# Kernel optimization log

Measured on AMD Instinct MI355X. Metric: run time of the kernel, lower is better.

## Reference

```python
import jax, jax.numpy as jnp
import numpy as np
import math
from jax.scipy.special import gammaln

B, H, W = 32, 960, 960
BLOCK = 96  # official NIQE/NRQM block size

# AGGD shape-parameter lookup table (same grid as torch impl: 0.2..10 step 0.001)
_GAM_NP = np.arange(0.2, 10.0 + 1e-6, 0.001, dtype=np.float64)
_RG_NP = np.array([math.exp(2.0 * math.lgamma(2.0 / g) - math.lgamma(1.0 / g) - math.lgamma(3.0 / g)) for g in _GAM_NP], dtype=np.float32)
GAM = jnp.asarray(_GAM_NP.astype(np.float32))
RGAM = jnp.asarray(_RG_NP)

def _gauss_kernel(size, sigma):
    ax = np.arange(size, dtype=np.float64) - (size - 1) / 2.0
    xx, yy = np.meshgrid(ax, ax)
    k = np.exp(-(xx ** 2 + yy ** 2) / (2.0 * sigma ** 2))
    return (k / k.sum()).astype(np.float32)

K7 = jnp.asarray(_gauss_kernel(7, 7.0 / 6.0))[None, None]  # MSCN window
K3 = jnp.asarray(_gauss_kernel(3, 0.5))[None, None]        # pyramid / downsample kernel

def _conv_same(x, k, edge_pad):
    ph = k.shape[-1] // 2
    mode = 'edge' if edge_pad else 'constant'
    x = jnp.pad(x, ((0, 0), (0, 0), (ph, ph), (ph, ph)), mode=mode)
    return jax.lax.conv_general_dilated(x, k, (1, 1), 'VALID', dimension_numbers=('NCHW', 'OIHW', 'NCHW'))

def _normalize(img):
    # MSCN: (img - mu) / (sigma + 1), replicate padding
    mu = _conv_same(img, K7, True)
    sigma = jnp.sqrt(jnp.abs(_conv_same(img * img, K7, True) - mu * mu))
    return (img - mu) / (sigma + 1.0)

def _downsample(img):
    # gaussian blur (3x3, sigma 0.5, zero same-pad) + stride-2 decimation
    return _conv_same(img, K3, False)[:, :, ::2, ::2]

def _aggd(x):
    # x: [b, nb, h, w]; vectorized AGGD parameter estimation over all blocks
    hw = (-2, -1)
    x2 = x * x
    ml = (x < 0).astype(x.dtype)
    mr = (x > 0).astype(x.dtype)
    cl = jnp.maximum(ml.sum(hw), 1.0)
    cr = jnp.maximum(mr.sum(hw), 1.0)
    lstd = jnp.sqrt((x2 * ml).sum(hw) / cl)
    rstd = jnp.sqrt((x2 * mr).sum(hw) / cr)
    gh = lstd / jnp.maximum(rstd, 1e-12)
    rhat = jnp.mean(jnp.abs(x), hw) ** 2 / jnp.maximum(jnp.mean(x2, hw), 1e-12)
    rhn = rhat * (gh ** 3 + 1.0) * (gh + 1.0) / ((gh * gh + 1.0) ** 2)
    idx = jnp.argmin(jnp.abs(RGAM - rhn[..., None]), axis=-1)  # table lookup
    alpha = GAM[idx]
    conv = jnp.exp(0.5 * (gammaln(1.0 / alpha) - gammaln(3.0 / alpha)))
    return alpha, lstd * conv, rstd * conv

def _features(blocks):
    # 18 features per block: AGGD of block + AGGD of 4 shifted products
    alpha, bl, br = _aggd(blocks)
    feats = [alpha, (bl + br) / 2.0]
    for shift in ((0, 1), (1, 0), (1, 1), (1, -1)):
        sb = jnp.roll(blocks, shift, axis=(2, 3))
        a, l, r = _aggd(blocks * sb)
        mean = (r - l) * jnp.exp(gammaln(2.0 / a) - gammaln(1.0 / a))
        feats += [a, mean, l, r]
    return jnp.stack(feats, axis=-1)  # [b, nb, 18]

def _blocks(x, bs):
    b, _, h, w = x.shape
    nh, nw = h // bs, w // bs
    x = x[:, 0].reshape(b, nh, bs, nw, bs).transpose(0, 1, 3, 2, 4)
    return x.reshape(b, nh * nw, bs, bs)

def setup_inputs() -> dict:
    key = jax.random.key(0)
    k1, k2, k3 = jax.random.split(key, 3)
    X = jax.random.uniform(k1, (B, 1, H, W), jnp.float32) * 255.0
    mu_pris = jax.random.normal(k2, (36,), jnp.float32)
    A = jax.random.normal(k3, (36, 36), jnp.float32)
    cov_pris = A @ A.T / 36.0 + jnp.eye(36, dtype=jnp.float32)  # SPD pristine covariance
    return {"X": X, "mu_pris": mu_pris, "cov_pris": cov_pris}

def reference(X, mu_pris, cov_pris):
    feats = []
    img = X
    for scale in (1, 2):
        xn = _normalize(img)
        feats.append(_features(_blocks(xn, BLOCK // scale)))  # [b, 100, 18]
        if scale == 1:
            img = _downsample(img)
    d = jnp.concatenate(feats, axis=-1)  # [b, nb, 36]
    mu_dist = d.mean(axis=1)  # [b, 36]
    c = d - mu_dist[:, None, :]
    cov_dist = jnp.einsum('bnf,bng->bfg', c, c) / (d.shape[1] - 1)
    invcov = jnp.linalg.pinv((cov_pris[None] + cov_dist) / 2.0)
    diff = mu_pris[None] - mu_dist
    q = jnp.einsum('bf,bfg,bg->b', diff, invcov, diff)
    return jnp.sqrt(jnp.maximum(q, 0.0))
```

## Files before the change

### kernel.cpp

```cpp
#include <hip/hip_runtime.h>
#include <hip/hip_fp16.h>
#include <math.h>

#define NTAB 9801
typedef unsigned int uint;

struct WParams { float w1[7]; float wd[3]; };

__device__ inline __half2 u2h2(uint u) { return __builtin_bit_cast(__half2, u); }
__device__ inline uint h22u(__half2 h) { return __builtin_bit_cast(uint, h); }
__device__ inline float flo(uint u) { return __low2float(u2h2(u)); }
__device__ inline float fhi(uint u) { return __high2float(u2h2(u)); }
__device__ inline uint pkmul(uint a, uint b) { return h22u(__hmul2(u2h2(a), u2h2(b))); }
__device__ inline uint pack2(float a, float b) {
    return h22u(__halves2half2(__float2half(a), __float2half(b)));
}
__device__ inline uint algn16(uint hi, uint lo) {
    return (uint)((((unsigned long long)hi << 32) | lo) >> 16);
}
typedef _Float16 h2v __attribute__((ext_vector_type(2)));
__device__ inline float fdot2f(uint a, uint b, float c) {
#if defined(__has_builtin) && __has_builtin(__builtin_amdgcn_fdot2)
    return __builtin_amdgcn_fdot2(__builtin_bit_cast(h2v, a), __builtin_bit_cast(h2v, b), c, false);
#else
    return c + flo(a) * flo(b) + fhi(a) * fhi(b);
#endif
}

template <int S, bool FUSE_DOWN, bool TABLES, typename TIN>
__global__ __launch_bounds__(256) void mscn_col_k(const TIN* __restrict__ src,
                                                  uint* __restrict__ xn_out,
                                                  __half* __restrict__ down_out,
                                                  WParams wp,
                                                  float* __restrict__ rgam,
                                                  float* __restrict__ gam) {
    constexpr int ROW_W = 132, H_IN = 34, H_OUT = 28;
    constexpr int NTX = (S + 255) / 256, NTY = (S + H_OUT - 1) / H_OUT;
    constexpr int NBLK = 32 * NTX * NTY;

    if constexpr (TABLES) {
        if (blockIdx.x >= (unsigned)NBLK) {
            int i = (blockIdx.x - NBLK) * 256 + threadIdx.x;
            if (i < NTAB) {
                double g = 0.2 + (double)i * 0.001;
                double v = exp(2.0 * lgamma(2.0 / g) - lgamma(1.0 / g) - lgamma(3.0 / g));
                rgam[i] = (float)v;
                gam[i]  = (float)g;
            }
            return;
        }
    }

    __shared__ uint tin[ROW_W * H_IN];

    const int tid = threadIdx.x;
    const int bid = blockIdx.x;
    const int b  = bid / (NTX * NTY);
    const int t2 = bid % (NTX * NTY);
    const int x0 = min((t2 / NTY) * 256, S - 256);
    const int y0 = min((t2 % NTY) * H_OUT, S - H_OUT);

    const float* w1 = wp.w1;
    uint wA[4], wB[4];
    wA[0] = pack2(w1[0], w1[1]); wA[1] = pack2(w1[2], w1[3]);
    wA[2] = pack2(w1[4], w1[5]); wA[3] = pack2(w1[6], 0.f);
    wB[0] = pack2(0.f, w1[0]);   wB[1] = pack2(w1[1], w1[2]);
    wB[2] = pack2(w1[3], w1[4]); wB[3] = pack2(w1[5], w1[6]);

    const TIN* img = src + (size_t)b * S * S;
    for (int i = tid; i < ROW_W * H_IN; i += 256) {
        int r = i / ROW_W, w = i - r * ROW_W;
        int gy = y0 + r - 3; gy = gy < 0 ? 0 : (gy >= S ? S - 1 : gy);
        int c0 = x0 + 2 * w - 3; c0 = c0 < 0 ? 0 : (c0 >= S ? S - 1 : c0);
        int c1 = (x0 + 2 * w - 2) < 0 ? 0 : ((x0 + 2 * w - 2) >= S ? S - 1 : x0 + 2 * w - 2);
        const TIN* rp = img + (size_t)gy * S;
        tin[i] = pack2((float)rp[c0], (float)rp[c1]);
    }
    __syncthreads();

    const int g = tid >> 7, c = tid & 127;
    const int R0 = g * 14;

    auto horiz = [&](int row, float& s1A, float& s2A, float& s1B, float& s2B) {
        const uint* pw = &tin[row * ROW_W + c];
        uint q0 = pw[0], q1 = pw[1], q2 = pw[2], q3 = pw[3];
        uint p0 = pkmul(q0, q0), p1 = pkmul(q1, q1), p2 = pkmul(q2, q2), p3 = pkmul(q3, q3);
        s1A = fdot2f(q3, wA[3], fdot2f(q2, wA[2], fdot2f(q1, wA[1], fdot2f(q0, wA[0], 0.f))));
        s2A = fdot2f(p3, wA[3], fdot2f(p2, wA[2], fdot2f(p1, wA[1], fdot2f(p0, wA[0], 0.f))));
        s1B = fdot2f(q3, wB[3], fdot2f(q2, wB[2], fdot2f(q1, wB[1], fdot2f(q0, wB[0], 0.f))));
        s2B = fdot2f(p3, wB[3], fdot2f(p2, wB[2], fdot2f(p1, wB[1], fdot2f(p0, wB[0], 0.f))));
    };

    float r1A[7], r2A[7], r1B[7], r2B[7];
#pragma unroll
    for (int ir = 0; ir < 6; ir++) horiz(R0 + ir, r1A[ir], r2A[ir], r1B[ir], r2B[ir]);

    uint* xnp = xn_out + ((((size_t)b * S + y0 + R0) * S + x0) >> 1) + c;
#pragma unroll
    for (int u = 0; u < 14; u++) {
        horiz(R0 + u + 6, r1A[(u + 6) % 7], r2A[(u + 6) % 7], r1B[(u + 6) % 7], r2B[(u + 6) % 7]);
        float s1a = 0.f, s2a = 0.f, s1b = 0.f, s2b = 0.f;
#pragma unroll
        for (int dy = 0; dy < 7; dy++) {
            s1a += w1[dy] * r1A[(u + dy) % 7];  s2a += w1[dy] * r2A[(u + dy) % 7];
            s1b += w1[dy] * r1B[(u + dy) % 7];  s2b += w1[dy] * r2B[(u + dy) % 7];
        }
        int row = R0 + u + 3;
        uint cw1 = tin[row * ROW_W + c + 1], cw2 = tin[row * ROW_W + c + 2];
        float v0a = fhi(cw1), v0b = flo(cw2);
        float xa = (v0a - s1a) / (sqrtf(fabsf(s2a - s1a * s1a)) + 1.f);
        float xb = (v0b - s1b) / (sqrtf(fabsf(s2b - s1b * s1b)) + 1.f);
        xnp[(size_t)u * (S / 2)] = pack2(xa, xb);
    }

    if constexpr (FUSE_DOWN) {
        const float* wd = wp.wd;
        const int d = tid & 127, hf = tid >> 7;
        const int Xd = x0 / 2 + d;
        const float mL = (x0 + 2 * d - 1 >= 0) ? 1.f : 0.f;
#pragma unroll
        for (int jj = 0; jj < 7; jj++) {
            int j = hf * 7 + jj;
            int Yd = y0 / 2 + j;
            float acc = 0.f;
#pragma unroll
            for (int a = 0; a < 3; a++) {
                int gy = 2 * Yd - 1 + a;
                if (gy < 0) continue;
                int tr = gy - y0 + 3;
                uint u1 = tin[tr * ROW_W + d + 1];
                uint u2 = tin[tr * ROW_W + d + 2];
                float rs = wd[0] * flo(u1) * mL + wd[1] * fhi(u1) + wd[2] * flo(u2);
                acc += wd[a] * rs;
            }
            down_out[((size_t)b * (S / 2) + Yd) * (S / 2) + Xd] = __float2half(acc);
        }
    }
}

template <int BS>
__global__ __launch_bounds__(256) void feat2_k(const __half* __restrict__ xnimg, int S,
                                               const float* __restrict__ rgam,
                                               const float* __restrict__ gam,
                                               float* __restrict__ dfeat, int foff) {
    constexpr int WROW = BS / 2;
    constexpr int NWORD = BS * BS / 2;
    constexpr int NITER = (NWORD + 255) / 256;
    __shared__ uint xs[NWORD];
    __shared__ float red[4 * 20];
    __shared__ float tot[20];

    const int tid = threadIdx.x;
    const int b   = blockIdx.x / 100;
    const int blk = blockIdx.x % 100;
    const int by  = (blk / 10) * BS;
    const int bx  = (blk % 10) * BS;

    const uint* gw = (const uint*)xnimg;
    for (int i = tid; i < NWORD; i += 256) {
        int y = i / WROW, w = i - y * WROW;
        xs[i] = gw[((((size_t)b * S + by + y) * S + bx) >> 1) + w];
    }
    __syncthreads();

    float ssq[5], sab[5], ssg[5];
    uint  cnt[5];
#pragma unroll
    for (int v = 0; v < 5; v++) { ssq[v] = sab[v] = ssg[v] = 0.f; cnt[v] = 0u; }

    const uint ONE2 = 0x3C003C00u;

    for (int k = 0; k < NITER; k++) {
        int idx = tid + k * 256;
        if (idx * 2 < BS * BS) {
            int p0 = idx * 2;
            int y = p0 / BS;
            int x = p0 - y * BS;
            int w0i = x >> 1;
            int wm = w0i ? w0i - 1 : WROW - 1;
            int wp = (w0i + 1 == WROW) ? 0 : w0i + 1;
            int ym1 = y ? y - 1 : BS - 1;
            int rb = y * WROW, rbm = ym1 * WROW;
            uint V0 = xs[rb + w0i];
            uint WL = xs[rb + wm];
            uint AL = xs[rbm + wm];
            uint AC = xs[rbm + w0i];
            uint AR = xs[rbm + wp];
            uint vv[5];
            vv[0] = V0;
            vv[1] = pkmul(V0, algn16(V0, WL));
            vv[2] = pkmul(V0, AC);
            vv[3] = pkmul(V0, algn16(AC, AL));
            vv[4] = pkmul(V0, algn16(AR, AC));
#pragma unroll
            for (int v = 0; v < 5; v++) {
                uint av = vv[v] & 0x7FFF7FFFu;
                ssq[v] = fdot2f(vv[v], vv[v], ssq[v]);
                sab[v] = fdot2f(av, ONE2, sab[v]);
                ssg[v] = fdot2f(vv[v], av, ssg[v]);
                cnt[v] += (vv[v] >> 15) & 0x00010001u;
            }
        }
    }

    const int wid = tid >> 6, lane = tid & 63;
#pragma unroll
    for (int v = 0; v < 5; v++) {
        float a = ssq[v], bb = sab[v], cc = ssg[v];
        float dd = (float)((cnt[v] & 0xFFFFu) + (cnt[v] >> 16));
        for (int off = 32; off >= 1; off >>= 1) {
            a += __shfl_down(a, off); bb += __shfl_down(bb, off);
            cc += __shfl_down(cc, off); dd += __shfl_down(dd, off);
        }
        if (lane == 0) {
            red[wid * 20 + v]      = a;
            red[wid * 20 + 5 + v]  = bb;
            red[wid * 20 + 10 + v] = cc;
            red[wid * 20 + 15 + v] = dd;
        }
    }
    __syncthreads();
    if (tid < 20) tot[tid] = red[tid] + red[20 + tid] + red[40 + tid] + red[60 + tid];
    __syncthreads();

    if (tid < 5) {
        const int v = tid;
        const float N = (float)(BS * BS);
        float ssqv = tot[v], sabv = tot[5 + v], ssgv = tot[10 + v], clv = tot[15 + v];
        float sql = fmaxf(0.5f * (ssqv - ssgv), 0.f);
        float sqr = fmaxf(0.5f * (ssqv + ssgv), 0.f);
        float cl = fmaxf(clv, 1.f), cr = fmaxf(N - clv, 1.f);
        float lstd = sqrtf(sql / cl), rstd = sqrtf(sqr / cr);
        float gh = lstd / fmaxf(rstd, 1e-12f);
        float mabs = sabv / N, msq = ssqv / N;
        float rhat = (mabs * mabs) / fmaxf(msq, 1e-12f);
        float gh2 = gh * gh;
        float target = rhat * (gh * gh2 + 1.f) * (gh + 1.f) / ((gh2 + 1.f) * (gh2 + 1.f));

        int lo = 0, hi = NTAB - 1, j = NTAB;
        while (lo <= hi) {
            int mid = (lo + hi) >> 1;
            if (rgam[mid] >= target) { j = mid; hi = mid - 1; } else lo = mid + 1;
        }
        int i0 = j > 0 ? j - 1 : 0;
        int i1 = j < NTAB ? j : NTAB - 1;
        float d0 = fabsf(rgam[i0] - target);
        float d1 = fabsf(rgam[i1] - target);
        int bi = (d1 < d0) ? i1 : i0;

        float alpha = gam[bi];
        float conv  = expf(0.5f * (lgammaf(1.f / alpha) - lgammaf(3.f / alpha)));
        float bl = lstd * conv, br = rstd * conv;
        float* outp = dfeat + ((size_t)b * 100 + blk) * 36 + foff;
        if (v == 0) {
            outp[0] = alpha;
            outp[1] = 0.5f * (bl + br);
        } else {
            float mean = (br - bl) * expf(lgammaf(2.f / alpha) - lgammaf(1.f / alpha));
            int base = 2 + (v - 1) * 4;
            outp[base + 0] = alpha; outp[base + 1] = mean;
            outp[base + 2] = bl;    outp[base + 3] = br;
        }
    }
}

__global__ __launch_bounds__(256) void final_k(const float* __restrict__ dfeat,
                                               const float* __restrict__ mu_pris,
                                               const float* __restrict__ cov_pris,
                                               float* __restrict__ out) {
    __shared__ float  ds[3600];
    __shared__ float  mu[36];
    __shared__ double M[36][37];
    __shared__ double rhs[36];
    __shared__ double qacc;
    const int b = blockIdx.x, tid = threadIdx.x;
    const float* src = dfeat + (size_t)b * 3600;
    for (int i = tid; i < 3600; i += 256) ds[i] = src[i];
    __syncthreads();
    if (tid < 36) {
        float s = 0.f;
        for (int n = 0; n < 100; n++) s += ds[n * 36 + tid];
        mu[tid] = s / 100.f;
    }
    __syncthreads();
    for (int i = tid; i < 3600; i += 256) ds[i] -= mu[i % 36];
    if (tid < 36) rhs[tid] = (double)mu_pris[tid] - (double)mu[tid];
    if (tid == 0) qacc = 0.0;
    __syncthreads();
    for (int e = tid; e < 1296; e += 256) {
        int f = e / 36, g = e % 36;
        float s = 0.f;
        for (int n = 0; n < 100; n++) s += ds[n * 36 + f] * ds[n * 36 + g];
        M[f][g] = 0.5 * ((double)cov_pris[e] + (double)(s / 99.f));
    }
    __syncthreads();
    for (int j = 0; j < 36; j++) {
        if (tid == 0) qacc += rhs[j] * rhs[j] / M[j][j];
        int i = j + 1 + tid;
        if (i < 36) {
            double L = M[i][j] / M[j][j];
            for (int k = j; k < 36; k++) M[i][k] -= L * M[j][k];
            rhs[i] -= L * rhs[j];
        }
        __syncthreads();
    }
    if (tid == 0) out[b] = sqrtf((float)(qacc > 0.0 ? qacc : 0.0));
}

static WParams make_weights() {
    WParams p;
    double wt[7], s = 0.0; const double sg = 7.0 / 6.0;
    for (int i = 0; i < 7; i++) { double d = i - 3; wt[i] = exp(-d * d / (2.0 * sg * sg)); s += wt[i]; }
    for (int i = 0; i < 7; i++) p.w1[i] = (float)(wt[i] / s);
    double e1 = exp(-2.0), sd = 1.0 + 2.0 * e1;
    p.wd[0] = p.wd[2] = (float)(e1 / sd);
    p.wd[1] = (float)(1.0 / sd);
    return p;
}

extern "C" void kernel_launch(void* const* d_in, const int* in_sizes, int n_in,
                              void* d_out, int out_size, void* d_ws, size_t ws_size,
                              hipStream_t stream) {
    const float* X        = (const float*)d_in[0];
    const float* mu_pris  = (const float*)d_in[1];
    const float* cov_pris = (const float*)d_in[2];
    float* out = (float*)d_out;

    char* ws = (char*)d_ws;
    float*  rgam   = (float*)(ws);
    float*  gam    = (float*)(ws + 39424);
    float*  dfeat  = (float*)(ws + 78848);
    __half* xn960  = (__half*)(ws + 539648);
    __half* img480 = (__half*)(ws + 59522048);
    __half* xn480  = (__half*)(ws + 74267648);

    WParams wp = make_weights();

    constexpr int NB960 = 32 * 4 * 35;
    constexpr int TBLB  = (NTAB + 255) / 256;
    mscn_col_k<960, true,  true,  float ><<<NB960 + TBLB, 256, 0, stream>>>(
        X, (uint*)xn960, img480, wp, rgam, gam);
    mscn_col_k<480, false, false, __half><<<32 * 36, 256, 0, stream>>>(
        img480, (uint*)xn480, nullptr, wp, rgam, gam);
    feat2_k<96><<<3200, 256, 0, stream>>>(xn960, 960, rgam, gam, dfeat, 0);
    feat2_k<48><<<3200, 256, 0, stream>>>(xn480, 480, rgam, gam, dfeat, 18);
    final_k<<<32, 256, 0, stream>>>(dfeat, mu_pris, cov_pris, out);
}
```

Before: 236.7 us.

## Enlarge MSCN row tiles, vectorize interior loads, use packed float2 and rcp

After: 223.2 us. -5.7%, faster.

```diff
diff --git a/kernel.cpp b/kernel.cpp
--- a/kernel.cpp
+++ b/kernel.cpp
@@ -4,37 +4,34 @@
 
 #define NTAB 9801
 typedef unsigned int uint;
+typedef float f2v __attribute__((ext_vector_type(2)));
+typedef _Float16 h2v __attribute__((ext_vector_type(2)));
 
 struct WParams { float w1[7]; float wd[3]; };
 
 __device__ inline __half2 u2h2(uint u) { return __builtin_bit_cast(__half2, u); }
-__device__ inline uint h22u(__half2 h) { return __builtin_bit_cast(uint, h); }
 __device__ inline float flo(uint u) { return __low2float(u2h2(u)); }
 __device__ inline float fhi(uint u) { return __high2float(u2h2(u)); }
-__device__ inline uint pkmul(uint a, uint b) { return h22u(__hmul2(u2h2(a), u2h2(b))); }
+__device__ inline uint pkmul(uint a, uint b) { return __builtin_bit_cast(uint, __hmul2(u2h2(a), u2h2(b))); }
 __device__ inline uint pack2(float a, float b) {
-    return h22u(__halves2half2(__float2half(a), __float2half(b)));
+    return __builtin_bit_cast(uint, __builtin_amdgcn_cvt_pkrtz(a, b));
 }
 __device__ inline uint algn16(uint hi, uint lo) {
     return (uint)((((unsigned long long)hi << 32) | lo) >> 16);
 }
-typedef _Float16 h2v __attribute__((ext_vector_type(2)));
 __device__ inline float fdot2f(uint a, uint b, float c) {
-#if defined(__has_builtin) && __has_builtin(__builtin_amdgcn_fdot2)
     return __builtin_amdgcn_fdot2(__builtin_bit_cast(h2v, a), __builtin_bit_cast(h2v, b), c, false);
-#else
-    return c + flo(a) * flo(b) + fhi(a) * fhi(b);
-#endif
-}
+}
+__device__ inline float rcpf(float x) { return __builtin_amdgcn_rcpf(x); }
 
 template <int S, bool FUSE_DOWN, bool TABLES, typename TIN>
-__global__ __launch_bounds__(256) void mscn_col_k(const TIN* __restrict__ src,
-                                                  uint* __restrict__ xn_out,
-                                                  __half* __restrict__ down_out,
-                                                  WParams wp,
-                                                  float* __restrict__ rgam,
-                                                  float* __restrict__ gam) {
-    constexpr int ROW_W = 132, H_IN = 34, H_OUT = 28;
+__global__ __launch_bounds__(256, 6) void mscn_col_k(const TIN* __restrict__ src,
+                                                     uint* __restrict__ xn_out,
+                                                     __half* __restrict__ down_out,
+                                                     WParams wp,
+                                                     float* __restrict__ rgam,
+                                                     float* __restrict__ gam) {
+    constexpr int ROW_W = 132, H_OUT = 42, H_IN = H_OUT + 6, RPT = H_OUT / 2;
     constexpr int NTX = (S + 255) / 256, NTY = (S + H_OUT - 1) / H_OUT;
     constexpr int NBLK = 32 * NTX * NTY;
 
@@ -62,54 +59,69 @@
 
     const float* w1 = wp.w1;
     uint wA[4], wB[4];
-    wA[0] = pack2(w1[0], w1[1]); wA[1] = pack2(w1[2], w1[3]);
-    wA[2] = pack2(w1[4], w1[5]); wA[3] = pack2(w1[6], 0.f);
-    wB[0] = pack2(0.f, w1[0]);   wB[1] = pack2(w1[1], w1[2]);
-    wB[2] = pack2(w1[3], w1[4]); wB[3] = pack2(w1[5], w1[6]);
+    wA[0] = pack2(0.f, w1[0]);   wA[1] = pack2(w1[1], w1[2]);
+    wA[2] = pack2(w1[3], w1[4]); wA[3] = pack2(w1[5], w1[6]);
+    wB[0] = pack2(w1[0], w1[1]); wB[1] = pack2(w1[2], w1[3]);
+    wB[2] = pack2(w1[4], w1[5]); wB[3] = pack2(w1[6], 0.f);
 
     const TIN* img = src + (size_t)b * S * S;
-    for (int i = tid; i < ROW_W * H_IN; i += 256) {
-        int r = i / ROW_W, w = i - r * ROW_W;
-        int gy = y0 + r - 3; gy = gy < 0 ? 0 : (gy >= S ? S - 1 : gy);
-        int c0 = x0 + 2 * w - 3; c0 = c0 < 0 ? 0 : (c0 >= S ? S - 1 : c0);
-        int c1 = (x0 + 2 * w - 2) < 0 ? 0 : ((x0 + 2 * w - 2) >= S ? S - 1 : x0 + 2 * w - 2);
-        const TIN* rp = img + (size_t)gy * S;
-        tin[i] = pack2((float)rp[c0], (float)rp[c1]);
+    const bool interior = (x0 >= 4) && (x0 <= S - 260) && (y0 >= 3) && (y0 <= S - H_IN + 3);
+
+    if (interior && sizeof(TIN) == 4) {
+        const float4* base = reinterpret_cast<const float4*>((const float*)img + (size_t)(y0 - 3) * S + (x0 - 4));
+        const int f4row = S / 4;
+        for (int i = tid; i < 66 * H_IN; i += 256) {
+            int r = i / 66, k = i - r * 66;
+            float4 v = base[(size_t)r * f4row + k];
+            tin[r * ROW_W + 2 * k]     = pack2(v.x, v.y);
+            tin[r * ROW_W + 2 * k + 1] = pack2(v.z, v.w);
+        }
+    } else {
+        for (int i = tid; i < ROW_W * H_IN; i += 256) {
+            int r = i / ROW_W, w = i - r * ROW_W;
+            int gy = y0 + r - 3; gy = gy < 0 ? 0 : (gy >= S ? S - 1 : gy);
+            int c0 = x0 - 4 + 2 * w; c0 = c0 < 0 ? 0 : (c0 >= S ? S - 1 : c0);
+            int c1 = x0 - 3 + 2 * w; c1 = c1 < 0 ? 0 : (c1 >= S ? S - 1 : c1);
+            const TIN* rp = img + (size_t)gy * S;
+            tin[i] = pack2((float)rp[c0], (float)rp[c1]);
+        }
     }
     __syncthreads();
 
     const int g = tid >> 7, c = tid & 127;
-    const int R0 = g * 14;
-
-    auto horiz = [&](int row, float& s1A, float& s2A, float& s1B, float& s2B) {
+    const int R0 = g * RPT;
+
+    auto horiz = [&](int row, f2v& o1, f2v& o2) {
         const uint* pw = &tin[row * ROW_W + c];
-        uint q0 = pw[0], q1 = pw[1], q2 = pw[2], q3 = pw[3];
-        uint p0 = pkmul(q0, q0), p1 = pkmul(q1, q1), p2 = pkmul(q2, q2), p3 = pkmul(q3, q3);
-        s1A = fdot2f(q3, wA[3], fdot2f(q2, wA[2], fdot2f(q1, wA[1], fdot2f(q0, wA[0], 0.f))));
-        s2A = fdot2f(p3, wA[3], fdot2f(p2, wA[2], fdot2f(p1, wA[1], fdot2f(p0, wA[0], 0.f))));
-        s1B = fdot2f(q3, wB[3], fdot2f(q2, wB[2], fdot2f(q1, wB[1], fdot2f(q0, wB[0], 0.f))));
-        s2B = fdot2f(p3, wB[3], fdot2f(p2, wB[2], fdot2f(p1, wB[1], fdot2f(p0, wB[0], 0.f))));
+        uint q0 = pw[0], q1 = pw[1], q2 = pw[2], q3 = pw[3], q4 = pw[4];
+        uint p0 = pkmul(q0, q0), p1 = pkmul(q1, q1), p2 = pkmul(q2, q2),
+             p3 = pkmul(q3, q3), p4 = pkmul(q4, q4);
+        float s1A = fdot2f(q3, wA[3], fdot2f(q2, wA[2], fdot2f(q1, wA[1], fdot2f(q0, wA[0], 0.f))));
+        float s2A = fdot2f(p3, wA[3], fdot2f(p2, wA[2], fdot2f(p1, wA[1], fdot2f(p0, wA[0], 0.f))));
+        float s1B = fdot2f(q4, wB[3], fdot2f(q3, wB[2], fdot2f(q2, wB[1], fdot2f(q1, wB[0], 0.f))));
+        float s2B = fdot2f(p4, wB[3], fdot2f(p3, wB[2], fdot2f(p2, wB[1], fdot2f(p1, wB[0], 0.f))));
+        o1 = (f2v){s1A, s1B};
+        o2 = (f2v){s2A, s2B};
     };
 
-    float r1A[7], r2A[7], r1B[7], r2B[7];
-#pragma unroll
-    for (int ir = 0; ir < 6; ir++) horiz(R0 + ir, r1A[ir], r2A[ir], r1B[ir], r2B[ir]);
+    f2v r1[7], r2[7];
+#pragma unroll
+    for (int ir = 0; ir < 6; ir++) horiz(R0 + ir, r1[ir], r2[ir]);
 
     uint* xnp = xn_out + ((((size_t)b * S + y0 + R0) * S + x0) >> 1) + c;
 #pragma unroll
-    for (int u = 0; u < 14; u++) {
-        horiz(R0 + u + 6, r1A[(u + 6) % 7], r2A[(u + 6) % 7], r1B[(u + 6) % 7], r2B[(u + 6) % 7]);
-        float s1a = 0.f, s2a = 0.f, s1b = 0.f, s2b = 0.f;
+    for (int u = 0; u < RPT; u++) {
+        horiz(R0 + u + 6, r1[(u + 6) % 7], r2[(u + 6) % 7]);
+        f2v a1 = (f2v)(0.f), a2 = (f2v)(0.f);
 #pragma unroll
         for (int dy = 0; dy < 7; dy++) {
-            s1a += w1[dy] * r1A[(u + dy) % 7];  s2a += w1[dy] * r2A[(u + dy) % 7];
-            s1b += w1[dy] * r1B[(u + dy) % 7];  s2b += w1[dy] * r2B[(u + dy) % 7];
-        }
-        int row = R0 + u + 3;
-        uint cw1 = tin[row * ROW_W + c + 1], cw2 = tin[row * ROW_W + c + 2];
-        float v0a = fhi(cw1), v0b = flo(cw2);
-        float xa = (v0a - s1a) / (sqrtf(fabsf(s2a - s1a * s1a)) + 1.f);
-        float xb = (v0b - s1b) / (sqrtf(fabsf(s2b - s1b * s1b)) + 1.f);
+            a1 += r1[(u + dy) % 7] * w1[dy];
+            a2 += r2[(u + dy) % 7] * w1[dy];
+        }
+        uint qc = tin[(R0 + u + 3) * ROW_W + c + 2];
+        float v0a = flo(qc), v0b = fhi(qc);
+        float xa = (v0a - a1.x) * rcpf(sqrtf(fabsf(a2.x - a1.x * a1.x)) + 1.f);
+        float xb = (v0b - a1.y) * rcpf(sqrtf(fabsf(a2.y - a1.y * a1.y)) + 1.f);
         xnp[(size_t)u * (S / 2)] = pack2(xa, xb);
     }
 
@@ -119,8 +131,9 @@
         const int Xd = x0 / 2 + d;
         const float mL = (x0 + 2 * d - 1 >= 0) ? 1.f : 0.f;
 #pragma unroll
-        for (int jj = 0; jj < 7; jj++) {
-            int j = hf * 7 + jj;
+        for (int jj = 0; jj <= RPT / 2; jj++) {
+            int j = 2 * jj + hf;
+            if (j >= RPT) continue;
             int Yd = y0 / 2 + j;
             float acc = 0.f;
 #pragma unroll
@@ -130,7 +143,7 @@
                 int tr = gy - y0 + 3;
                 uint u1 = tin[tr * ROW_W + d + 1];
                 uint u2 = tin[tr * ROW_W + d + 2];
-                float rs = wd[0] * flo(u1) * mL + wd[1] * fhi(u1) + wd[2] * flo(u2);
+                float rs = wd[0] * fhi(u1) * mL + wd[1] * flo(u2) + wd[2] * fhi(u2);
                 acc += wd[a] * rs;
             }
             down_out[((size_t)b * (S / 2) + Yd) * (S / 2) + Xd] = __float2half(acc);
@@ -336,11 +349,11 @@
 
     WParams wp = make_weights();
 
-    constexpr int NB960 = 32 * 4 * 35;
+    constexpr int NB960 = 32 * 4 * 23;
     constexpr int TBLB  = (NTAB + 255) / 256;
     mscn_col_k<960, true,  true,  float ><<<NB960 + TBLB, 256, 0, stream>>>(
         X, (uint*)xn960, img480, wp, rgam, gam);
-    mscn_col_k<480, false, false, __half><<<32 * 36, 256, 0, stream>>>(
+    mscn_col_k<480, false, false, __half><<<32 * 2 * 12, 256, 0, stream>>>(
         img480, (uint*)xn480, nullptr, wp, rgam, gam);
     feat2_k<96><<<3200, 256, 0, stream>>>(xn960, 960, rgam, gam, dfeat, 0);
     feat2_k<48><<<3200, 256, 0, stream>>>(xn480, 480, rgam, gam, dfeat, 18);
```
